# Kernel optimization log

Hardware: AMD Instinct MI355X
Metric: run time of the kernel (lower is better)

The kernel has to match this reference:

```python
import jax, jax.numpy as jnp
import numpy as np
import math

B, L, D = 2, 4096, 1024
K = D // 4


def _rotor(angles):
    # angles: [..., 6] -> scalar part s: [...], bivector part: [..., 6]
    mag = jnp.maximum(jnp.linalg.norm(angles, axis=-1), 1e-8)
    s = jnp.cos(mag)
    biv = (jnp.sin(mag) / mag)[..., None] * angles
    return s, biv


def _apply_rotor(s, biv, v):
    # s: [...], biv: [..., 6] (e12,e13,e14,e23,e24,e34), v: [..., 4]
    t12, t13, t14, t23, t24, t34 = (biv[..., i] for i in range(6))
    v1, v2, v3, v4 = (v[..., i] for i in range(4))
    s2 = s * s
    ts = 2.0 * s
    v1n = v1 * (s2 - t12 * t12 - t13 * t13 - t14 * t14) + ts * (v2 * t12 + v3 * t13 + v4 * t14)
    v2n = v2 * (s2 - t12 * t12 - t23 * t23 - t24 * t24) + ts * (-v1 * t12 + v3 * t23 + v4 * t24)
    v3n = v3 * (s2 - t13 * t13 - t23 * t23 - t34 * t34) + ts * (-v1 * t13 - v2 * t23 + v4 * t34)
    v4n = v4 * (s2 - t14 * t14 - t24 * t24 - t34 * t34) + ts * (-v1 * t14 - v2 * t24 - v3 * t34)
    return jnp.stack([v1n, v2n, v3n, v4n], axis=-1)


def _forward(x, wk1, bk1, wk2, bk2, wq1, bq1, wq2, bq2, wv, bv, ln_g, ln_b, wo, bo):
    b, l, d = x.shape
    k = d // 4
    gelu = lambda t: jax.nn.gelu(t, approximate=False)  # torch nn.GELU default = exact
    half_pi = math.pi / 2
    key_angles = (jnp.tanh(gelu(x @ wk1 + bk1) @ wk2 + bk2) * half_pi).reshape(b, l, k, 6)
    query_angles = (jnp.tanh(gelu(x @ wq1 + bq1) @ wq2 + bq2) * half_pi).reshape(b, l, k, 6)
    value = (x @ wv + bv).reshape(b, l, k, 4)
    ks, kb = _rotor(key_angles)
    qs, qb = _rotor(query_angles)
    rotated_value = _apply_rotor(ks, kb, value)          # [B,L,K,4]
    memory = jnp.cumsum(rotated_value, axis=1)            # running sum over sequence
    retrieved = _apply_rotor(qs, -qb, memory)             # reversed query rotor
    retrieved = retrieved.reshape(b, l, d)
    norm = jnp.sqrt(jnp.arange(1, l + 1, dtype=x.dtype))[None, :, None]
    r = retrieved / norm
    # LayerNorm (eps=1e-5) then Linear
    mu = jnp.mean(r, axis=-1, keepdims=True)
    var = jnp.mean((r - mu) ** 2, axis=-1, keepdims=True)
    rn = (r - mu) / jnp.sqrt(var + 1e-5) * ln_g + ln_b
    return x + rn @ wo + bo


def setup_inputs() -> dict:
    key = jax.random.key(0)
    ks = jax.random.split(key, 8)
    lin = lambda k, fi, fo: (jax.random.normal(k, (fi, fo), jnp.float32) * 0.02)
    return {
        "x": jax.random.normal(ks[0], (B, L, D), jnp.float32),
        "wk1": lin(ks[1], D, D), "bk1": jnp.zeros((D,), jnp.float32),
        "wk2": lin(ks[2], D, K * 6), "bk2": jnp.zeros((K * 6,), jnp.float32),
        "wq1": lin(ks[3], D, D), "bq1": jnp.zeros((D,), jnp.float32),
        "wq2": lin(ks[4], D, K * 6), "bq2": jnp.zeros((K * 6,), jnp.float32),
        "wv": lin(ks[5], D, D), "bv": jnp.zeros((D,), jnp.float32),
        "ln_g": jnp.ones((D,), jnp.float32), "ln_b": jnp.zeros((D,), jnp.float32),
        "wo": lin(ks[6], D, D), "bo": jnp.zeros((D,), jnp.float32),
    }


def reference(x, wk1, bk1, wk2, bk2, wq1, bq1, wq2, bq2, wv, bv, ln_g, ln_b, wo, bo):
    return _forward(x, wk1, bk1, wk2, bk2, wq1, bq1, wq2, bq2, wv, bv, ln_g, ln_b, wo, bo)
```

## Files before the change

kernel.cpp:

```cpp
#include <hip/hip_runtime.h>
#include <hip/hip_bf16.h>
#include <math.h>

#define D_DIM 1024
#define L_DIM 4096
#define B_DIM 2
#define K_DIM 256
#define N6    1536
#define M_ROWS 8192
#define CHUNKS 256
#define CHUNK_LEN 16
#define HALF_PI 1.57079632679489662f

typedef __attribute__((ext_vector_type(8))) short short8;
typedef __attribute__((ext_vector_type(4))) float f32x4;
typedef unsigned short us;

__device__ __forceinline__ void gload_lds16(const void* g, void* l) {
    __builtin_amdgcn_global_load_lds(
        (const __attribute__((address_space(1))) unsigned int*)g,
        (__attribute__((address_space(3))) unsigned int*)l,
        16, 0, 0);
}
__device__ __forceinline__ float bf2f(us u) {
    union { unsigned int i; float f; } c; c.i = ((unsigned int)u) << 16; return c.f;
}
__device__ __forceinline__ us f2bf(float v) {
    __hip_bfloat16 h = __float2bfloat16(v);
    return *(us*)&h;
}
__device__ __forceinline__ float tanh_fast(float x) {
    return 1.0f - 2.0f / (1.0f + __expf(2.0f * x));
}
__device__ __forceinline__ float gelu_fast(float x) {
    return x / (1.0f + __expf(-1.5957691216057308f * x * (1.0f + 0.044715f * x * x)));
}

__device__ __forceinline__ void rotor_from_angles(const float a[6], float& s, float b[6]) {
    float m2 = a[0]*a[0] + a[1]*a[1] + a[2]*a[2] + a[3]*a[3] + a[4]*a[4] + a[5]*a[5];
    float mag = fmaxf(sqrtf(m2), 1e-8f);
    s = __cosf(mag);
    float f = __sinf(mag) / mag;
    #pragma unroll
    for (int i = 0; i < 6; ++i) b[i] = f * a[i];
}
__device__ __forceinline__ void apply_rotor(float s, const float b[6], const float v[4], float o[4]) {
    float t12 = b[0], t13 = b[1], t14 = b[2], t23 = b[3], t24 = b[4], t34 = b[5];
    float v1 = v[0], v2 = v[1], v3 = v[2], v4 = v[3];
    float s2 = s * s;
    float ts = 2.0f * s;
    o[0] = v1 * (s2 - t12*t12 - t13*t13 - t14*t14) + ts * ( v2*t12 + v3*t13 + v4*t14);
    o[1] = v2 * (s2 - t12*t12 - t23*t23 - t24*t24) + ts * (-v1*t12 + v3*t23 + v4*t24);
    o[2] = v3 * (s2 - t13*t13 - t23*t23 - t34*t34) + ts * (-v1*t13 - v2*t23 + v4*t34);
    o[3] = v4 * (s2 - t14*t14 - t24*t24 - t34*t34) + ts * (-v1*t14 - v2*t24 - v3*t34);
}

__global__ __launch_bounds__(256)
void pack_b4(const float* __restrict__ w0, const float* __restrict__ w1,
             const float* __restrict__ w2, const float* __restrict__ w3,
             us* __restrict__ o0, us* __restrict__ o1,
             us* __restrict__ o2, us* __restrict__ o3, int Kd, int N)
{
    const float* W = (blockIdx.z == 0) ? w0 : (blockIdx.z == 1) ? w1 : (blockIdx.z == 2) ? w2 : w3;
    us* O = (blockIdx.z == 0) ? o0 : (blockIdx.z == 1) ? o1 : (blockIdx.z == 2) ? o2 : o3;
    if (W == nullptr) return;
    int nf = blockIdx.x;
    int kt = blockIdx.y * 4 + (threadIdx.x >> 6);
    int l = threadIdx.x & 63;
    int n = nf * 16 + (l & 15);
    int k0 = kt * 32 + (l >> 4) * 8;
    union { us u[8]; uint4 v; } pk;
    #pragma unroll
    for (int j = 0; j < 8; ++j)
        pk.u[j] = f2bf(W[(size_t)(k0 + j) * N + n]);
    *(uint4*)(O + ((size_t)nf * (Kd >> 5) + kt) * 512 + l * 8) = pk.v;
}

__global__ __launch_bounds__(256)
void cvt_bf16_kernel(const float* __restrict__ in, us* __restrict__ out)
{
    size_t i = ((size_t)blockIdx.x * 256 + threadIdx.x) * 8;
    float4 v0 = *(const float4*)(in + i);
    float4 v1 = *(const float4*)(in + i + 4);
    union { us u[8]; uint4 v; } pk;
    pk.u[0] = f2bf(v0.x); pk.u[1] = f2bf(v0.y); pk.u[2] = f2bf(v0.z); pk.u[3] = f2bf(v0.w);
    pk.u[4] = f2bf(v1.x); pk.u[5] = f2bf(v1.y); pk.u[6] = f2bf(v1.z); pk.u[7] = f2bf(v1.w);
    *(uint4*)(out + i) = pk.v;
}

__device__ __forceinline__ int xcd_swz(int bid, int nwg) {
    int cpx = nwg >> 3;
    return (bid & 7) * cpx + (bid >> 3);
}


#define GBAR()  do { __builtin_amdgcn_s_barrier(); __builtin_amdgcn_sched_barrier(0); } while (0)

__device__ __forceinline__ void gemm128_core(
    const us* __restrict__ Ab, const us* __restrict__ Bp, int Kd, int bn,
    short* lds, f32x4 (&acc)[4][4])
{
    const int tid = threadIdx.x;
    const int l = tid & 63, w = tid >> 6;
    const int wr = w >> 1, wc = w & 1;
    const int fr = l & 15, fq = l >> 4;
    const int nkt = Kd >> 5;

    #pragma unroll
    for (int i = 0; i < 4; ++i)
        #pragma unroll
        for (int j = 0; j < 4; ++j)
            acc[i][j] = (f32x4){0.f, 0.f, 0.f, 0.f};

    const us* bptr[4];
    #pragma unroll
    for (int ni = 0; ni < 4; ++ni)
        bptr[ni] = Bp + ((size_t)((bn >> 4) + wc * 4 + ni) * nkt) * 512 + l * 8;

    const int sr = tid >> 2, su = tid & 3;
    const int slu = su ^ ((sr >> 1) & 3);
    const us* gA0 = Ab + (size_t)sr * Kd + slu * 8;
    const us* gA1 = gA0 + (size_t)64 * Kd;

    const int swu = (fq ^ ((fr >> 1) & 3)) * 8;
    const int arow = (wr * 64 + fr) * 32 + swu;

    gload_lds16(gA0,      lds + tid * 8);
    gload_lds16(gA1,      lds + 2048 + tid * 8);
    gload_lds16(gA0 + 32, lds + 4096 + tid * 8);
    gload_lds16(gA1 + 32, lds + 6144 + tid * 8);
    gload_lds16(gA0 + 64, lds + 8192 + tid * 8);
    gload_lds16(gA1 + 64, lds + 10240 + tid * 8);
    asm volatile("s_waitcnt vmcnt(4)" ::: "memory");
    short8 bA[4], bB[4];
    #pragma unroll
    for (int ni = 0; ni < 4; ++ni) bA[ni] = *(const short8*)(bptr[ni]);
    #pragma unroll
    for (int ni = 0; ni < 4; ++ni) bB[ni] = *(const short8*)(bptr[ni] + 512);
    GBAR();

    for (int t = 0; t < nkt; t += 2) {
        {
            const int cb = (t % 3) * 4096;
            const int sb = ((t + 2) % 3) * 4096;
            const int tp = (t + 2 < nkt) ? (t + 2) : (nkt - 1);
            short8 a[4];
            #pragma unroll
            for (int mi = 0; mi < 4; ++mi)
                a[mi] = *(const short8*)(lds + cb + arow + mi * 512);
            gload_lds16(gA0 + tp * 32, lds + sb + tid * 8);
            gload_lds16(gA1 + tp * 32, lds + sb + 2048 + tid * 8);
            __builtin_amdgcn_s_setprio(1);
            #pragma unroll
            for (int mi = 0; mi < 4; ++mi)
                #pragma unroll
                for (int ni = 0; ni < 4; ++ni)
                    acc[mi][ni] = __builtin_amdgcn_mfma_f32_16x16x32_bf16(bA[ni], a[mi], acc[mi][ni], 0, 0, 0);
            __builtin_amdgcn_sched_barrier(0);
            __builtin_amdgcn_s_setprio(0);
            #pragma unroll
            for (int ni = 0; ni < 4; ++ni)
                bA[ni] = *(const short8*)(bptr[ni] + (size_t)tp * 512);
            asm volatile("s_waitcnt vmcnt(6)" ::: "memory");
            GBAR();
        }
        {
            const int t1 = t + 1;
            const int cb = (t1 % 3) * 4096;
            const int sb = ((t1 + 2) % 3) * 4096;
            const int tp = (t1 + 2 < nkt) ? (t1 + 2) : (nkt - 1);
            short8 a[4];
            #pragma unroll
            for (int mi = 0; mi < 4; ++mi)
                a[mi] = *(const short8*)(lds + cb + arow + mi * 512);
            gload_lds16(gA0 + tp * 32, lds + sb + tid * 8);
            gload_lds16(gA1 + tp * 32, lds + sb + 2048 + tid * 8);
            __builtin_amdgcn_s_setprio(1);
            #pragma unroll
            for (int mi = 0; mi < 4; ++mi)
                #pragma unroll
                for (int ni = 0; ni < 4; ++ni)
                    acc[mi][ni] = __builtin_amdgcn_mfma_f32_16x16x32_bf16(bB[ni], a[mi], acc[mi][ni], 0, 0, 0);
            __builtin_amdgcn_sched_barrier(0);
            __builtin_amdgcn_s_setprio(0);
            #pragma unroll
            for (int ni = 0; ni < 4; ++ni)
                bB[ni] = *(const short8*)(bptr[ni] + (size_t)tp * 512);
            asm volatile("s_waitcnt vmcnt(6)" ::: "memory");
            GBAR();
        }
    }
}

__global__ __launch_bounds__(256, 3)
void gemm_fused3(const us* __restrict__ xb,
                 const us* __restrict__ w0p, const us* __restrict__ w1p, const us* __restrict__ w2p,
                 const float* __restrict__ b0, const float* __restrict__ b1, const float* __restrict__ b2,
                 us* __restrict__ o0, us* __restrict__ o1, us* __restrict__ o2)
{
    __shared__ short lds[12288];
    const int wg = xcd_swz(blockIdx.x, 1536);
    const int bm = (wg / 24) * 128;
    const int col = wg % 24;
    const int r = col >> 3;
    const int bn = (col & 7) * 128;
    const us* Bp = (r == 0) ? w0p : (r == 1) ? w1p : w2p;
    const float* bias = (r == 0) ? b0 : (r == 1) ? b1 : b2;
    us* outp = (r == 0) ? o0 : (r == 1) ? o1 : o2;
    f32x4 acc[4][4];
    gemm128_core(xb + (size_t)bm * D_DIM, Bp, D_DIM, bn, lds, acc);
    const int l = threadIdx.x & 63, w = threadIdx.x >> 6;
    const int wr = w >> 1, wc = w & 1, fr = l & 15, fq = l >> 4;
    #pragma unroll
    for (int mi = 0; mi < 4; ++mi) {
        int row = bm + wr * 64 + mi * 16 + fr;
        #pragma unroll
        for (int ni = 0; ni < 4; ++ni) {
            int c0 = bn + wc * 64 + ni * 16 + fq * 4;
            float4 bs = *(const float4*)(bias + c0);
            float v0 = acc[mi][ni][0] + bs.x, v1 = acc[mi][ni][1] + bs.y;
            float v2 = acc[mi][ni][2] + bs.z, v3 = acc[mi][ni][3] + bs.w;
            if (r < 2) { v0 = gelu_fast(v0); v1 = gelu_fast(v1); v2 = gelu_fast(v2); v3 = gelu_fast(v3); }
            ushort4 pk; pk.x = f2bf(v0); pk.y = f2bf(v1); pk.z = f2bf(v2); pk.w = f2bf(v3);
            *(ushort4*)(outp + (size_t)row * D_DIM + c0) = pk;
        }
    }
}

__global__ __launch_bounds__(256, 3)
void gemm_angles(const us* __restrict__ Hk, const us* __restrict__ Hq,
                 const us* __restrict__ wk2p, const us* __restrict__ wq2p,
                 const float* __restrict__ bk2, const float* __restrict__ bq2,
                 us* __restrict__ ak, us* __restrict__ aq)
{
    __shared__ short lds[12288];
    const int wg = xcd_swz(blockIdx.x, 1536);
    const int z = wg / 768;
    const int rem = wg % 768;
    const int bm = (rem / 12) * 128;
    const int bn = (rem % 12) * 128;
    const us* A  = z ? Hq : Hk;
    const us* Bp = z ? wq2p : wk2p;
    const float* bias = z ? bq2 : bk2;
    us* outp = z ? aq : ak;
    f32x4 acc[4][4];
    gemm128_core(A + (size_t)bm * D_DIM, Bp, D_DIM, bn, lds, acc);
    const int l = threadIdx.x & 63, w = threadIdx.x >> 6;
    const int wr = w >> 1, wc = w & 1, fr = l & 15, fq = l >> 4;
    #pragma unroll
    for (int mi = 0; mi < 4; ++mi) {
        int row = bm + wr * 64 + mi * 16 + fr;
        #pragma unroll
        for (int ni = 0; ni < 4; ++ni) {
            int c0 = bn + wc * 64 + ni * 16 + fq * 4;
            float4 bs = *(const float4*)(bias + c0);
            ushort4 pk;
            pk.x = f2bf(tanh_fast(acc[mi][ni][0] + bs.x) * HALF_PI);
            pk.y = f2bf(tanh_fast(acc[mi][ni][1] + bs.y) * HALF_PI);
            pk.z = f2bf(tanh_fast(acc[mi][ni][2] + bs.z) * HALF_PI);
            pk.w = f2bf(tanh_fast(acc[mi][ni][3] + bs.w) * HALF_PI);
            *(ushort4*)(outp + (size_t)row * N6 + c0) = pk;
        }
    }
}

__global__ __launch_bounds__(256, 3)
void gemm_final(const us* __restrict__ rn, const us* __restrict__ wop,
                const float* __restrict__ bo, const float* __restrict__ x,
                float* __restrict__ out)
{
    __shared__ short lds[12288];
    const int wg = xcd_swz(blockIdx.x, 512);
    const int bm = (wg / 8) * 128;
    const int bn = (wg % 8) * 128;
    f32x4 acc[4][4];
    gemm128_core(rn + (size_t)bm * D_DIM, wop, D_DIM, bn, lds, acc);
    const int l = threadIdx.x & 63, w = threadIdx.x >> 6;
    const int wr = w >> 1, wc = w & 1, fr = l & 15, fq = l >> 4;
    #pragma unroll
    for (int mi = 0; mi < 4; ++mi) {
        int row = bm + wr * 64 + mi * 16 + fr;
        #pragma unroll
        for (int ni = 0; ni < 4; ++ni) {
            int c0 = bn + wc * 64 + ni * 16 + fq * 4;
            size_t off = (size_t)row * D_DIM + c0;
            float4 bs = *(const float4*)(bo + c0);
            float4 rx = *(const float4*)(x + off);
            float4 o;
            o.x = acc[mi][ni][0] + bs.x + rx.x;
            o.y = acc[mi][ni][1] + bs.y + rx.y;
            o.z = acc[mi][ni][2] + bs.z + rx.z;
            o.w = acc[mi][ni][3] + bs.w + rx.w;
            *(float4*)(out + off) = o;
        }
    }
}

__global__ __launch_bounds__(256)
void rot_chunk_sum(us* __restrict__ value, const us* __restrict__ ak,
                   float4* __restrict__ sums)
{
    int bc = blockIdx.x;
    int b = bc >> 8, c = bc & 255;
    int k = threadIdx.x;
    float4 acc = make_float4(0.f, 0.f, 0.f, 0.f);
    size_t row0 = (size_t)b * L_DIM + c * CHUNK_LEN;
    for (int i = 0; i < CHUNK_LEN; ++i) {
        size_t row = row0 + i;
        ushort4 uv = *(const ushort4*)(value + row * D_DIM + k * 4);
        const unsigned int* ap = (const unsigned int*)(ak + row * N6 + k * 6);
        unsigned int a0 = ap[0], a1 = ap[1], a2 = ap[2];
        float a[6] = { bf2f(a0 & 0xffff), bf2f(a0 >> 16), bf2f(a1 & 0xffff),
                       bf2f(a1 >> 16), bf2f(a2 & 0xffff), bf2f(a2 >> 16) };
        float s, bb[6];
        rotor_from_angles(a, s, bb);
        float v[4] = {bf2f(uv.x), bf2f(uv.y), bf2f(uv.z), bf2f(uv.w)}, o[4];
        apply_rotor(s, bb, v, o);
        ushort4 pkr;
        pkr.x = f2bf(o[0]); pkr.y = f2bf(o[1]); pkr.z = f2bf(o[2]); pkr.w = f2bf(o[3]);
        *(ushort4*)(value + row * D_DIM + k * 4) = pkr;
        acc.x += bf2f(pkr.x); acc.y += bf2f(pkr.y); acc.z += bf2f(pkr.z); acc.w += bf2f(pkr.w);
    }
    sums[(size_t)bc * 256 + k] = acc;
}

__global__ __launch_bounds__(256)
void scan_chunks_kernel(const float4* __restrict__ sums, float4* __restrict__ carry)
{
    int b = blockIdx.x >> 8;
    int k = blockIdx.x & 255;
    int c = threadIdx.x;
    __shared__ float4 sh[CHUNKS];
    float4 v = sums[((size_t)(b * CHUNKS + c)) * 256 + k];
    sh[c] = v;
    __syncthreads();
    for (int off = 1; off < CHUNKS; off <<= 1) {
        float4 t = make_float4(0.f, 0.f, 0.f, 0.f);
        if (c >= off) t = sh[c - off];
        __syncthreads();
        v.x += t.x; v.y += t.y; v.z += t.z; v.w += t.w;
        sh[c] = v;
        __syncthreads();
    }
    float4 ex = make_float4(0.f, 0.f, 0.f, 0.f);
    if (c > 0) ex = sh[c - 1];
    carry[((size_t)(b * CHUNKS + c)) * 256 + k] = ex;
}

__global__ __launch_bounds__(256)
void scan_apply_ln(const us* __restrict__ value, const us* __restrict__ aq,
                   const float4* __restrict__ carry,
                   const float* __restrict__ g, const float* __restrict__ bta,
                   us* __restrict__ rn)
{
    int bc = blockIdx.x;
    int b = bc >> 8, c = bc & 255;
    int k = threadIdx.x;
    int wv = k >> 6, lane = k & 63;
    float4 run = carry[(size_t)bc * 256 + k];
    float4 gv = *(const float4*)(g + k * 4);
    float4 bv = *(const float4*)(bta + k * 4);
    __shared__ float reds[4], redq[4];
    for (int i = 0; i < CHUNK_LEN; ++i) {
        int l = c * CHUNK_LEN + i;
        size_t row = (size_t)b * L_DIM + l;
        ushort4 uv = *(const ushort4*)(value + row * D_DIM + k * 4);
        run.x += bf2f(uv.x); run.y += bf2f(uv.y); run.z += bf2f(uv.z); run.w += bf2f(uv.w);
        const unsigned int* aqp = (const unsigned int*)(aq + row * N6 + k * 6);
        unsigned int qa0 = aqp[0], qa1 = aqp[1], qa2 = aqp[2];
        float aq6[6] = { bf2f(qa0 & 0xffff), bf2f(qa0 >> 16), bf2f(qa1 & 0xffff),
                         bf2f(qa1 >> 16), bf2f(qa2 & 0xffff), bf2f(qa2 >> 16) };
        float qs, qb[6];
        rotor_from_angles(aq6, qs, qb);
        #pragma unroll
        for (int t = 0; t < 6; ++t) qb[t] = -qb[t];
        float mem[4] = {run.x, run.y, run.z, run.w}, o2[4];
        apply_rotor(qs, qb, mem, o2);
        float inv = rsqrtf((float)(l + 1));
        o2[0] *= inv; o2[1] *= inv; o2[2] *= inv; o2[3] *= inv;
        float sm = o2[0] + o2[1] + o2[2] + o2[3];
        float qm = o2[0]*o2[0] + o2[1]*o2[1] + o2[2]*o2[2] + o2[3]*o2[3];
        #pragma unroll
        for (int off = 1; off < 64; off <<= 1) {
            sm += __shfl_xor(sm, off);
            qm += __shfl_xor(qm, off);
        }
        if (lane == 0) { reds[wv] = sm; redq[wv] = qm; }
        __syncthreads();
        sm = reds[0] + reds[1] + reds[2] + reds[3];
        qm = redq[0] + redq[1] + redq[2] + redq[3];
        float mu = sm * (1.0f / 1024.0f);
        float var = qm * (1.0f / 1024.0f) - mu * mu;
        float rstd = rsqrtf(var + 1e-5f);
        ushort4 pk;
        pk.x = f2bf((o2[0] - mu) * rstd * gv.x + bv.x);
        pk.y = f2bf((o2[1] - mu) * rstd * gv.y + bv.y);
        pk.z = f2bf((o2[2] - mu) * rstd * gv.z + bv.z);
        pk.w = f2bf((o2[3] - mu) * rstd * gv.w + bv.w);
        *(ushort4*)(rn + row * D_DIM + k * 4) = pk;
        __syncthreads();
    }
}

extern "C" void kernel_launch(void* const* d_in, const int* in_sizes, int n_in,
                              void* d_out, int out_size, void* d_ws, size_t ws_size,
                              hipStream_t stream)
{
    const float* x   = (const float*)d_in[0];
    const float* wk1 = (const float*)d_in[1];
    const float* bk1 = (const float*)d_in[2];
    const float* wk2 = (const float*)d_in[3];
    const float* bk2 = (const float*)d_in[4];
    const float* wq1 = (const float*)d_in[5];
    const float* bq1 = (const float*)d_in[6];
    const float* wq2 = (const float*)d_in[7];
    const float* bq2 = (const float*)d_in[8];
    const float* wv  = (const float*)d_in[9];
    const float* bv  = (const float*)d_in[10];
    const float* lng = (const float*)d_in[11];
    const float* lnb = (const float*)d_in[12];
    const float* wo  = (const float*)d_in[13];
    const float* bo  = (const float*)d_in[14];
    float* out = (float*)d_out;

    char* ws = (char*)d_ws;
    us* xb    = (us*)(ws);
    us* Hk    = (us*)(ws + (16ull  << 20));
    us* Hq    = (us*)(ws + (32ull  << 20));
    us* val   = (us*)(ws + (48ull  << 20));
    us* ak    = (us*)(ws + (64ull  << 20));
    us* aq    = (us*)(ws + (88ull  << 20));
    float4* sums  = (float4*)(ws + (112ull << 20));
    float4* carry = (float4*)(ws + (114ull << 20));
    us* wk1p  = (us*)(ws + (116ull << 20));
    us* wq1p  = (us*)(ws + (118ull << 20));
    us* wvp   = (us*)(ws + (120ull << 20));
    us* wop   = (us*)(ws + (122ull << 20));
    us* wk2p  = (us*)(ws + (124ull << 20));
    us* wq2p  = (us*)(ws + (127ull << 20));
    us* rn    = xb;

    dim3 blk(256);
    pack_b4<<<dim3(D_DIM / 16, D_DIM / 128, 4), blk, 0, stream>>>(
        wk1, wq1, wv, wo, wk1p, wq1p, wvp, wop, D_DIM, D_DIM);
    pack_b4<<<dim3(N6 / 16, D_DIM / 128, 2), blk, 0, stream>>>(
        wk2, wq2, nullptr, nullptr, wk2p, wq2p, nullptr, nullptr, D_DIM, N6);
    cvt_bf16_kernel<<<dim3(M_ROWS * D_DIM / (256 * 8)), blk, 0, stream>>>(x, xb);

    gemm_fused3<<<dim3(1536), blk, 0, stream>>>(
        xb, wk1p, wq1p, wvp, bk1, bq1, bv, Hk, Hq, val);
    gemm_angles<<<dim3(1536), blk, 0, stream>>>(
        Hk, Hq, wk2p, wq2p, bk2, bq2, ak, aq);
    rot_chunk_sum<<<dim3(B_DIM * CHUNKS), blk, 0, stream>>>(val, ak, sums);
    scan_chunks_kernel<<<dim3(B_DIM * K_DIM), blk, 0, stream>>>(sums, carry);
    scan_apply_ln<<<dim3(B_DIM * CHUNKS), blk, 0, stream>>>(val, aq, carry, lng, lnb, rn);
    gemm_final<<<dim3(512), blk, 0, stream>>>(rn, wop, bo, x, out);
}
```

Baseline: 229.3 us.

## Replace 128x128 GEMMs with 256x256 eight-wave tiles using transposed bf16 weights

The first-layer fused GEMM and the angle GEMM move from a 128x128, 4-wave tile to a 256x256, 8-wave tile. The new tile double-buffers K=64 slices in 128KB of dynamic LDS with an XOR swizzle, and interleaves four MFMA quadrants with staged global-to-LDS loads. Weights are now transposed and converted into plain N-major bf16 by a shared-memory transpose kernel, replacing the fragment-packed layout. The aim is more operand reuse and fewer global/LDS loads per FLOP. The costs are a 384-block grid that fills 256 CUs unevenly, occupancy limited to about one block per CU by LDS, and hipFuncSetAttribute calls on every launch.

```diff
diff --git a/kernel.cpp b/kernel.cpp
--- a/kernel.cpp
+++ b/kernel.cpp
@@ -56,14 +56,29 @@
 }
 
 __global__ __launch_bounds__(256)
-void pack_b4(const float* __restrict__ w0, const float* __restrict__ w1,
-             const float* __restrict__ w2, const float* __restrict__ w3,
-             us* __restrict__ o0, us* __restrict__ o1,
-             us* __restrict__ o2, us* __restrict__ o3, int Kd, int N)
+void transpose_cvt4(const float* __restrict__ w0, const float* __restrict__ w1,
+                    const float* __restrict__ w2, const float* __restrict__ w3,
+                    us* __restrict__ o0, us* __restrict__ o1,
+                    us* __restrict__ o2, us* __restrict__ o3, int Kd, int N)
 {
     const float* W = (blockIdx.z == 0) ? w0 : (blockIdx.z == 1) ? w1 : (blockIdx.z == 2) ? w2 : w3;
-    us* O = (blockIdx.z == 0) ? o0 : (blockIdx.z == 1) ? o1 : (blockIdx.z == 2) ? o2 : o3;
+    us* Wt = (blockIdx.z == 0) ? o0 : (blockIdx.z == 1) ? o1 : (blockIdx.z == 2) ? o2 : o3;
     if (W == nullptr) return;
+    __shared__ float sh[32][33];
+    int n0 = blockIdx.x * 32, k0 = blockIdx.y * 32;
+    int tx = threadIdx.x & 31, ty = threadIdx.x >> 5;
+    #pragma unroll
+    for (int i = 0; i < 32; i += 8)
+        sh[ty + i][tx] = W[(size_t)(k0 + ty + i) * N + n0 + tx];
+    __syncthreads();
+    #pragma unroll
+    for (int i = 0; i < 32; i += 8)
+        Wt[(size_t)(n0 + ty + i) * Kd + k0 + tx] = f2bf(sh[tx][ty + i]);
+}
+
+__global__ __launch_bounds__(256)
+void pack_b1(const float* __restrict__ W, us* __restrict__ O, int Kd, int N)
+{
     int nf = blockIdx.x;
     int kt = blockIdx.y * 4 + (threadIdx.x >> 6);
     int l = threadIdx.x & 63;
@@ -93,8 +108,214 @@
     return (bid & 7) * cpx + (bid >> 3);
 }
 
-
 #define GBAR()  do { __builtin_amdgcn_s_barrier(); __builtin_amdgcn_sched_barrier(0); } while (0)
+#define LGKM0() do { asm volatile("s_waitcnt lgkmcnt(0)" ::: "memory"); __builtin_amdgcn_sched_barrier(0); } while (0)
+
+
+__device__ __forceinline__ void gemm256_core(
+    const us* __restrict__ Ab, const us* __restrict__ Bb, int Kd,
+    short* lds, f32x4 (&acc)[8][4])
+{
+    const int tid = threadIdx.x;
+    const int l = tid & 63, w = tid >> 6;
+    const int wm = w >> 2, wn = w & 3;
+    const int fr = l & 15, fq = l >> 4, fr7 = fr & 7;
+    const int w16 = w * 16, sr = l >> 3;
+    const int gu = (l & 7) ^ sr;
+    const int nkt = Kd >> 6;
+
+    #pragma unroll
+    for (int i = 0; i < 8; ++i)
+        #pragma unroll
+        for (int j = 0; j < 4; ++j)
+            acc[i][j] = (f32x4){0.f, 0.f, 0.f, 0.f};
+
+    short* buf0 = lds;
+    short* buf1 = lds + 32768;
+
+    auto STAGE = [&](const us* gbase, int GR, int kt, short* half) {
+        gload_lds16(gbase + (size_t)(GR + w16 + sr) * Kd + kt * 64 + gu * 8,
+                    half + w16 * 64 + l * 8);
+        gload_lds16(gbase + (size_t)(GR + w16 + 8 + sr) * Kd + kt * 64 + gu * 8,
+                    half + (w16 + 8) * 64 + l * 8);
+    };
+
+    STAGE(Ab, 0,   0, buf0 + 0);
+    STAGE(Ab, 128, 0, buf0 + 8192);
+    STAGE(Bb, 0,   0, buf0 + 16384);
+    STAGE(Bb, 128, 0, buf0 + 24576);
+    STAGE(Bb, 0,   1, buf1 + 16384);
+    STAGE(Ab, 0,   1, buf1 + 0);
+    asm volatile("s_waitcnt vmcnt(4)" ::: "memory");
+    GBAR();
+
+    const int aoff = wm * 8192;
+    const int boff = 16384 + (wn >> 1) * 8192;
+    const int brow0 = (wn & 1) * 64;
+
+    short8 aR[4][2], bLo[2][2], bHi[2][2];
+
+    for (int t = 0; t < nkt; ++t) {
+        short* cb = (t & 1) ? buf1 : buf0;
+        short* ob = (t & 1) ? buf0 : buf1;
+        const int t1 = (t + 1 < nkt) ? t + 1 : nkt - 1;
+        const int t2 = (t + 2 < nkt) ? t + 2 : nkt - 1;
+        short* abuf = cb + aoff;
+        short* bbuf = cb + boff;
+
+        #pragma unroll
+        for (int mi = 0; mi < 4; ++mi)
+            #pragma unroll
+            for (int ks = 0; ks < 2; ++ks)
+                aR[mi][ks] = *(const short8*)(abuf + (mi * 16 + fr) * 64 + (((ks * 4 + fq) ^ fr7) * 8));
+        #pragma unroll
+        for (int ni = 0; ni < 2; ++ni)
+            #pragma unroll
+            for (int ks = 0; ks < 2; ++ks)
+                bLo[ni][ks] = *(const short8*)(bbuf + (brow0 + ni * 16 + fr) * 64 + (((ks * 4 + fq) ^ fr7) * 8));
+        STAGE(Ab, 128, t1, ob + 8192);
+        __builtin_amdgcn_s_barrier();
+        LGKM0();
+        __builtin_amdgcn_s_setprio(1);
+        #pragma unroll
+        for (int mi = 0; mi < 4; ++mi)
+            #pragma unroll
+            for (int ni = 0; ni < 2; ++ni)
+                #pragma unroll
+                for (int ks = 0; ks < 2; ++ks)
+                    acc[mi][ni] = __builtin_amdgcn_mfma_f32_16x16x32_bf16(bLo[ni][ks], aR[mi][ks], acc[mi][ni], 0, 0, 0);
+        __builtin_amdgcn_sched_barrier(0);
+        __builtin_amdgcn_s_setprio(0);
+        GBAR();
+
+        #pragma unroll
+        for (int ni = 0; ni < 2; ++ni)
+            #pragma unroll
+            for (int ks = 0; ks < 2; ++ks)
+                bHi[ni][ks] = *(const short8*)(bbuf + (brow0 + (ni + 2) * 16 + fr) * 64 + (((ks * 4 + fq) ^ fr7) * 8));
+        STAGE(Bb, 128, t1, ob + 24576);
+        __builtin_amdgcn_s_barrier();
+        LGKM0();
+        __builtin_amdgcn_s_setprio(1);
+        #pragma unroll
+        for (int mi = 0; mi < 4; ++mi)
+            #pragma unroll
+            for (int ni = 0; ni < 2; ++ni)
+                #pragma unroll
+                for (int ks = 0; ks < 2; ++ks)
+                    acc[mi][ni + 2] = __builtin_amdgcn_mfma_f32_16x16x32_bf16(bHi[ni][ks], aR[mi][ks], acc[mi][ni + 2], 0, 0, 0);
+        __builtin_amdgcn_sched_barrier(0);
+        __builtin_amdgcn_s_setprio(0);
+        GBAR();
+
+        #pragma unroll
+        for (int mi = 0; mi < 4; ++mi)
+            #pragma unroll
+            for (int ks = 0; ks < 2; ++ks)
+                aR[mi][ks] = *(const short8*)(abuf + ((mi + 4) * 16 + fr) * 64 + (((ks * 4 + fq) ^ fr7) * 8));
+        STAGE(Bb, 0, t2, cb + 16384);
+        __builtin_amdgcn_s_barrier();
+        LGKM0();
+        __builtin_amdgcn_s_setprio(1);
+        #pragma unroll
+        for (int mi = 0; mi < 4; ++mi)
+            #pragma unroll
+            for (int ni = 0; ni < 2; ++ni)
+                #pragma unroll
+                for (int ks = 0; ks < 2; ++ks)
+                    acc[mi + 4][ni + 2] = __builtin_amdgcn_mfma_f32_16x16x32_bf16(bHi[ni][ks], aR[mi][ks], acc[mi + 4][ni + 2], 0, 0, 0);
+        __builtin_amdgcn_sched_barrier(0);
+        __builtin_amdgcn_s_setprio(0);
+        GBAR();
+
+        STAGE(Ab, 0, t2, cb + 0);
+        GBAR();
+        __builtin_amdgcn_s_setprio(1);
+        #pragma unroll
+        for (int mi = 0; mi < 4; ++mi)
+            #pragma unroll
+            for (int ni = 0; ni < 2; ++ni)
+                #pragma unroll
+                for (int ks = 0; ks < 2; ++ks)
+                    acc[mi + 4][ni] = __builtin_amdgcn_mfma_f32_16x16x32_bf16(bLo[ni][ks], aR[mi][ks], acc[mi + 4][ni], 0, 0, 0);
+        __builtin_amdgcn_sched_barrier(0);
+        __builtin_amdgcn_s_setprio(0);
+        asm volatile("s_waitcnt vmcnt(4)" ::: "memory");
+        GBAR();
+    }
+}
+
+__global__ __launch_bounds__(512, 2)
+void gemm256_fused3(const us* __restrict__ xb,
+                    const us* __restrict__ w0t, const us* __restrict__ w1t, const us* __restrict__ w2t,
+                    const float* __restrict__ b0, const float* __restrict__ b1, const float* __restrict__ b2,
+                    us* __restrict__ o0, us* __restrict__ o1, us* __restrict__ o2)
+{
+    extern __shared__ short lds[];
+    const int wg = xcd_swz(blockIdx.x, 384);
+    const int bm = (wg / 12) * 256;
+    const int col = wg % 12;
+    const int r = col >> 2;
+    const int bn = (col & 3) * 256;
+    const us* Bt = (r == 0) ? w0t : (r == 1) ? w1t : w2t;
+    const float* bias = (r == 0) ? b0 : (r == 1) ? b1 : b2;
+    us* outp = (r == 0) ? o0 : (r == 1) ? o1 : o2;
+    f32x4 acc[8][4];
+    gemm256_core(xb + (size_t)bm * D_DIM, Bt + (size_t)bn * D_DIM, D_DIM, lds, acc);
+    const int l = threadIdx.x & 63, w = threadIdx.x >> 6;
+    const int wm = w >> 2, wn = w & 3, fr = l & 15, fq = l >> 4;
+    #pragma unroll
+    for (int mi = 0; mi < 8; ++mi) {
+        int row = bm + wm * 128 + mi * 16 + fr;
+        #pragma unroll
+        for (int ni = 0; ni < 4; ++ni) {
+            int c0 = bn + wn * 64 + ni * 16 + fq * 4;
+            float4 bs = *(const float4*)(bias + c0);
+            float v0 = acc[mi][ni][0] + bs.x, v1 = acc[mi][ni][1] + bs.y;
+            float v2 = acc[mi][ni][2] + bs.z, v3 = acc[mi][ni][3] + bs.w;
+            if (r < 2) { v0 = gelu_fast(v0); v1 = gelu_fast(v1); v2 = gelu_fast(v2); v3 = gelu_fast(v3); }
+            ushort4 pk; pk.x = f2bf(v0); pk.y = f2bf(v1); pk.z = f2bf(v2); pk.w = f2bf(v3);
+            *(ushort4*)(outp + (size_t)row * D_DIM + c0) = pk;
+        }
+    }
+}
+
+__global__ __launch_bounds__(512, 2)
+void gemm256_angles(const us* __restrict__ Hk, const us* __restrict__ Hq,
+                    const us* __restrict__ wk2t, const us* __restrict__ wq2t,
+                    const float* __restrict__ bk2, const float* __restrict__ bq2,
+                    us* __restrict__ ak, us* __restrict__ aq)
+{
+    extern __shared__ short lds[];
+    const int wg = xcd_swz(blockIdx.x, 384);
+    const int z = wg / 192;
+    const int rem = wg % 192;
+    const int bm = (rem / 6) * 256;
+    const int bn = (rem % 6) * 256;
+    const us* A  = z ? Hq : Hk;
+    const us* Bt = z ? wq2t : wk2t;
+    const float* bias = z ? bq2 : bk2;
+    us* outp = z ? aq : ak;
+    f32x4 acc[8][4];
+    gemm256_core(A + (size_t)bm * D_DIM, Bt + (size_t)bn * D_DIM, D_DIM, lds, acc);
+    const int l = threadIdx.x & 63, w = threadIdx.x >> 6;
+    const int wm = w >> 2, wn = w & 3, fr = l & 15, fq = l >> 4;
+    #pragma unroll
+    for (int mi = 0; mi < 8; ++mi) {
+        int row = bm + wm * 128 + mi * 16 + fr;
+        #pragma unroll
+        for (int ni = 0; ni < 4; ++ni) {
+            int c0 = bn + wn * 64 + ni * 16 + fq * 4;
+            float4 bs = *(const float4*)(bias + c0);
+            ushort4 pk;
+            pk.x = f2bf(tanh_fast(acc[mi][ni][0] + bs.x) * HALF_PI);
+            pk.y = f2bf(tanh_fast(acc[mi][ni][1] + bs.y) * HALF_PI);
+            pk.z = f2bf(tanh_fast(acc[mi][ni][2] + bs.z) * HALF_PI);
+            pk.w = f2bf(tanh_fast(acc[mi][ni][3] + bs.w) * HALF_PI);
+            *(ushort4*)(outp + (size_t)row * N6 + c0) = pk;
+        }
+    }
+}
 
 __device__ __forceinline__ void gemm128_core(
     const us* __restrict__ Ab, const us* __restrict__ Bp, int Kd, int bn,
@@ -188,78 +409,6 @@
                 bB[ni] = *(const short8*)(bptr[ni] + (size_t)tp * 512);
             asm volatile("s_waitcnt vmcnt(6)" ::: "memory");
             GBAR();
-        }
-    }
-}
-
-__global__ __launch_bounds__(256, 3)
-void gemm_fused3(const us* __restrict__ xb,
-                 const us* __restrict__ w0p, const us* __restrict__ w1p, const us* __restrict__ w2p,
-                 const float* __restrict__ b0, const float* __restrict__ b1, const float* __restrict__ b2,
-                 us* __restrict__ o0, us* __restrict__ o1, us* __restrict__ o2)
-{
-    __shared__ short lds[12288];
-    const int wg = xcd_swz(blockIdx.x, 1536);
-    const int bm = (wg / 24) * 128;
-    const int col = wg % 24;
-    const int r = col >> 3;
-    const int bn = (col & 7) * 128;
-    const us* Bp = (r == 0) ? w0p : (r == 1) ? w1p : w2p;
-    const float* bias = (r == 0) ? b0 : (r == 1) ? b1 : b2;
-    us* outp = (r == 0) ? o0 : (r == 1) ? o1 : o2;
-    f32x4 acc[4][4];
-    gemm128_core(xb + (size_t)bm * D_DIM, Bp, D_DIM, bn, lds, acc);
-    const int l = threadIdx.x & 63, w = threadIdx.x >> 6;
-    const int wr = w >> 1, wc = w & 1, fr = l & 15, fq = l >> 4;
-    #pragma unroll
-    for (int mi = 0; mi < 4; ++mi) {
-        int row = bm + wr * 64 + mi * 16 + fr;
-        #pragma unroll
-        for (int ni = 0; ni < 4; ++ni) {
-            int c0 = bn + wc * 64 + ni * 16 + fq * 4;
-            float4 bs = *(const float4*)(bias + c0);
-            float v0 = acc[mi][ni][0] + bs.x, v1 = acc[mi][ni][1] + bs.y;
-            float v2 = acc[mi][ni][2] + bs.z, v3 = acc[mi][ni][3] + bs.w;
-            if (r < 2) { v0 = gelu_fast(v0); v1 = gelu_fast(v1); v2 = gelu_fast(v2); v3 = gelu_fast(v3); }
-            ushort4 pk; pk.x = f2bf(v0); pk.y = f2bf(v1); pk.z = f2bf(v2); pk.w = f2bf(v3);
-            *(ushort4*)(outp + (size_t)row * D_DIM + c0) = pk;
-        }
-    }
-}
-
-__global__ __launch_bounds__(256, 3)
-void gemm_angles(const us* __restrict__ Hk, const us* __restrict__ Hq,
-                 const us* __restrict__ wk2p, const us* __restrict__ wq2p,
-                 const float* __restrict__ bk2, const float* __restrict__ bq2,
-                 us* __restrict__ ak, us* __restrict__ aq)
-{
-    __shared__ short lds[12288];
-    const int wg = xcd_swz(blockIdx.x, 1536);
-    const int z = wg / 768;
-    const int rem = wg % 768;
-    const int bm = (rem / 12) * 128;
-    const int bn = (rem % 12) * 128;
-    const us* A  = z ? Hq : Hk;
-    const us* Bp = z ? wq2p : wk2p;
-    const float* bias = z ? bq2 : bk2;
-    us* outp = z ? aq : ak;
-    f32x4 acc[4][4];
-    gemm128_core(A + (size_t)bm * D_DIM, Bp, D_DIM, bn, lds, acc);
-    const int l = threadIdx.x & 63, w = threadIdx.x >> 6;
-    const int wr = w >> 1, wc = w & 1, fr = l & 15, fq = l >> 4;
-    #pragma unroll
-    for (int mi = 0; mi < 4; ++mi) {
-        int row = bm + wr * 64 + mi * 16 + fr;
-        #pragma unroll
-        for (int ni = 0; ni < 4; ++ni) {
-            int c0 = bn + wc * 64 + ni * 16 + fq * 4;
-            float4 bs = *(const float4*)(bias + c0);
-            ushort4 pk;
-            pk.x = f2bf(tanh_fast(acc[mi][ni][0] + bs.x) * HALF_PI);
-            pk.y = f2bf(tanh_fast(acc[mi][ni][1] + bs.y) * HALF_PI);
-            pk.z = f2bf(tanh_fast(acc[mi][ni][2] + bs.z) * HALF_PI);
-            pk.w = f2bf(tanh_fast(acc[mi][ni][3] + bs.w) * HALF_PI);
-            *(ushort4*)(outp + (size_t)row * N6 + c0) = pk;
         }
     }
 }
@@ -432,25 +581,32 @@
     us* aq    = (us*)(ws + (88ull  << 20));
     float4* sums  = (float4*)(ws + (112ull << 20));
     float4* carry = (float4*)(ws + (114ull << 20));
-    us* wk1p  = (us*)(ws + (116ull << 20));
-    us* wq1p  = (us*)(ws + (118ull << 20));
-    us* wvp   = (us*)(ws + (120ull << 20));
+    us* wk1t  = (us*)(ws + (116ull << 20));
+    us* wq1t  = (us*)(ws + (118ull << 20));
+    us* wvt   = (us*)(ws + (120ull << 20));
     us* wop   = (us*)(ws + (122ull << 20));
-    us* wk2p  = (us*)(ws + (124ull << 20));
-    us* wq2p  = (us*)(ws + (127ull << 20));
+    us* wk2t  = (us*)(ws + (124ull << 20));
+    us* wq2t  = (us*)(ws + (127ull << 20));
     us* rn    = xb;
 
+    hipFuncSetAttribute((const void*)gemm256_fused3,
+                        hipFuncAttributeMaxDynamicSharedMemorySize, 131072);
+    hipFuncSetAttribute((const void*)gemm256_angles,
+                        hipFuncAttributeMaxDynamicSharedMemorySize, 131072);
+
     dim3 blk(256);
-    pack_b4<<<dim3(D_DIM / 16, D_DIM / 128, 4), blk, 0, stream>>>(
-        wk1, wq1, wv, wo, wk1p, wq1p, wvp, wop, D_DIM, D_DIM);
-    pack_b4<<<dim3(N6 / 16, D_DIM / 128, 2), blk, 0, stream>>>(
-        wk2, wq2, nullptr, nullptr, wk2p, wq2p, nullptr, nullptr, D_DIM, N6);
+    transpose_cvt4<<<dim3(D_DIM / 32, D_DIM / 32, 3), blk, 0, stream>>>(
+        wk1, wq1, wv, nullptr, wk1t, wq1t, wvt, nullptr, D_DIM, D_DIM);
+    transpose_cvt4<<<dim3(N6 / 32, D_DIM / 32, 2), blk, 0, stream>>>(
+        wk2, wq2, nullptr, nullptr, wk2t, wq2t, nullptr, nullptr, D_DIM, N6);
+    pack_b1<<<dim3(D_DIM / 16, D_DIM / 128), blk, 0, stream>>>(wo, wop, D_DIM, D_DIM);
     cvt_bf16_kernel<<<dim3(M_ROWS * D_DIM / (256 * 8)), blk, 0, stream>>>(x, xb);
 
-    gemm_fused3<<<dim3(1536), blk, 0, stream>>>(
-        xb, wk1p, wq1p, wvp, bk1, bq1, bv, Hk, Hq, val);
-    gemm_angles<<<dim3(1536), blk, 0, stream>>>(
-        Hk, Hq, wk2p, wq2p, bk2, bq2, ak, aq);
+    dim3 blk512(512);
+    gemm256_fused3<<<dim3(384), blk512, 131072, stream>>>(
+        xb, wk1t, wq1t, wvt, bk1, bq1, bv, Hk, Hq, val);
+    gemm256_angles<<<dim3(384), blk512, 131072, stream>>>(
+        Hk, Hq, wk2t, wq2t, bk2, bq2, ak, aq);
     rot_chunk_sum<<<dim3(B_DIM * CHUNKS), blk, 0, stream>>>(val, ak, sums);
     scan_chunks_kernel<<<dim3(B_DIM * K_DIM), blk, 0, stream>>>(sums, carry);
     scan_apply_ln<<<dim3(B_DIM * CHUNKS), blk, 0, stream>>>(val, aq, carry, lng, lnb, rn);
```

New measurement: 241.8 us. +5.5%, slower.

## Double GEMM K-step to 64 per LDS stage with wider swizzle

Applied to the files above, without the earlier changes.

The shared bf16 GEMM core now stages 64-wide K tiles of A in LDS instead of 32, so each triple-buffered stage holds 128x64 elements. Each stage issues two MFMA sweeps, and B fragments are prefetched two K-subtiles at a time. The goal is to halve the number of barriers and loop iterations per K, amortising synchronisation and load-issue overhead. In exchange LDS per block doubles to 48KB, which may limit occupancy under launch_bounds(256,3), and more registers are needed for the B fragments.

```diff
diff --git a/kernel.cpp b/kernel.cpp
--- a/kernel.cpp
+++ b/kernel.cpp
@@ -93,8 +93,8 @@
     return (bid & 7) * cpx + (bid >> 3);
 }
 
-
 #define GBAR()  do { __builtin_amdgcn_s_barrier(); __builtin_amdgcn_sched_barrier(0); } while (0)
+
 
 __device__ __forceinline__ void gemm128_core(
     const us* __restrict__ Ab, const us* __restrict__ Bp, int Kd, int bn,
@@ -104,7 +104,8 @@
     const int l = tid & 63, w = tid >> 6;
     const int wr = w >> 1, wc = w & 1;
     const int fr = l & 15, fq = l >> 4;
-    const int nkt = Kd >> 5;
+    const int nkt = Kd >> 6;
+    const int nt32 = Kd >> 5;
 
     #pragma unroll
     for (int i = 0; i < 4; ++i)
@@ -115,78 +116,114 @@
     const us* bptr[4];
     #pragma unroll
     for (int ni = 0; ni < 4; ++ni)
-        bptr[ni] = Bp + ((size_t)((bn >> 4) + wc * 4 + ni) * nkt) * 512 + l * 8;
-
-    const int sr = tid >> 2, su = tid & 3;
-    const int slu = su ^ ((sr >> 1) & 3);
-    const us* gA0 = Ab + (size_t)sr * Kd + slu * 8;
-    const us* gA1 = gA0 + (size_t)64 * Kd;
-
-    const int swu = (fq ^ ((fr >> 1) & 3)) * 8;
-    const int arow = (wr * 64 + fr) * 32 + swu;
-
-    gload_lds16(gA0,      lds + tid * 8);
-    gload_lds16(gA1,      lds + 2048 + tid * 8);
-    gload_lds16(gA0 + 32, lds + 4096 + tid * 8);
-    gload_lds16(gA1 + 32, lds + 6144 + tid * 8);
-    gload_lds16(gA0 + 64, lds + 8192 + tid * 8);
-    gload_lds16(gA1 + 64, lds + 10240 + tid * 8);
+        bptr[ni] = Bp + ((size_t)((bn >> 4) + wc * 4 + ni) * nt32) * 512 + l * 8;
+
+    const us* gA[4];
+    int dsto[4];
+    #pragma unroll
+    for (int j = 0; j < 4; ++j) {
+        int idx = tid + j * 256;
+        int row = idx >> 3, u = idx & 7;
+        int lu = u ^ (row & 7);
+        gA[j] = Ab + (size_t)row * Kd + lu * 8;
+        dsto[j] = idx * 8;
+    }
+
+    const int sw0 = ((fq) ^ (fr & 7)) * 8;
+    const int sw1 = ((4 + fq) ^ (fr & 7)) * 8;
+    const int rowb = (wr * 64 + fr) * 64;
+
+    #pragma unroll
+    for (int j = 0; j < 4; ++j) gload_lds16(gA[j], lds + dsto[j]);
+    #pragma unroll
+    for (int j = 0; j < 4; ++j) gload_lds16(gA[j] + 64, lds + 8192 + dsto[j]);
+    short8 bA[4][2], bB[4][2];
+    #pragma unroll
+    for (int ni = 0; ni < 4; ++ni)
+        #pragma unroll
+        for (int ks = 0; ks < 2; ++ks) {
+            bA[ni][ks] = *(const short8*)(bptr[ni] + (0 + ks) * 512);
+            bB[ni][ks] = *(const short8*)(bptr[ni] + (2 + ks) * 512);
+        }
     asm volatile("s_waitcnt vmcnt(4)" ::: "memory");
-    short8 bA[4], bB[4];
-    #pragma unroll
-    for (int ni = 0; ni < 4; ++ni) bA[ni] = *(const short8*)(bptr[ni]);
-    #pragma unroll
-    for (int ni = 0; ni < 4; ++ni) bB[ni] = *(const short8*)(bptr[ni] + 512);
     GBAR();
 
     for (int t = 0; t < nkt; t += 2) {
         {
-            const int cb = (t % 3) * 4096;
-            const int sb = ((t + 2) % 3) * 4096;
+            const int cb = (t % 3) * 8192;
+            const int sb = ((t + 2) % 3) * 8192;
             const int tp = (t + 2 < nkt) ? (t + 2) : (nkt - 1);
             short8 a[4];
             #pragma unroll
             for (int mi = 0; mi < 4; ++mi)
-                a[mi] = *(const short8*)(lds + cb + arow + mi * 512);
-            gload_lds16(gA0 + tp * 32, lds + sb + tid * 8);
-            gload_lds16(gA1 + tp * 32, lds + sb + 2048 + tid * 8);
+                a[mi] = *(const short8*)(lds + cb + rowb + mi * 1024 + sw0);
+            #pragma unroll
+            for (int j = 0; j < 4; ++j)
+                gload_lds16(gA[j] + tp * 64, lds + sb + dsto[j]);
             __builtin_amdgcn_s_setprio(1);
             #pragma unroll
             for (int mi = 0; mi < 4; ++mi)
                 #pragma unroll
                 for (int ni = 0; ni < 4; ++ni)
-                    acc[mi][ni] = __builtin_amdgcn_mfma_f32_16x16x32_bf16(bA[ni], a[mi], acc[mi][ni], 0, 0, 0);
+                    acc[mi][ni] = __builtin_amdgcn_mfma_f32_16x16x32_bf16(bA[ni][0], a[mi], acc[mi][ni], 0, 0, 0);
             __builtin_amdgcn_sched_barrier(0);
             __builtin_amdgcn_s_setprio(0);
             #pragma unroll
+            for (int mi = 0; mi < 4; ++mi)
+                a[mi] = *(const short8*)(lds + cb + rowb + mi * 1024 + sw1);
+            __builtin_amdgcn_s_setprio(1);
+            #pragma unroll
+            for (int mi = 0; mi < 4; ++mi)
+                #pragma unroll
+                for (int ni = 0; ni < 4; ++ni)
+                    acc[mi][ni] = __builtin_amdgcn_mfma_f32_16x16x32_bf16(bA[ni][1], a[mi], acc[mi][ni], 0, 0, 0);
+            __builtin_amdgcn_sched_barrier(0);
+            __builtin_amdgcn_s_setprio(0);
+            #pragma unroll
             for (int ni = 0; ni < 4; ++ni)
-                bA[ni] = *(const short8*)(bptr[ni] + (size_t)tp * 512);
-            asm volatile("s_waitcnt vmcnt(6)" ::: "memory");
+                #pragma unroll
+                for (int ks = 0; ks < 2; ++ks)
+                    bA[ni][ks] = *(const short8*)(bptr[ni] + (size_t)(2 * tp + ks) * 512);
+            asm volatile("s_waitcnt vmcnt(12)" ::: "memory");
             GBAR();
         }
         {
             const int t1 = t + 1;
-            const int cb = (t1 % 3) * 4096;
-            const int sb = ((t1 + 2) % 3) * 4096;
+            const int cb = (t1 % 3) * 8192;
+            const int sb = ((t1 + 2) % 3) * 8192;
             const int tp = (t1 + 2 < nkt) ? (t1 + 2) : (nkt - 1);
             short8 a[4];
             #pragma unroll
             for (int mi = 0; mi < 4; ++mi)
-                a[mi] = *(const short8*)(lds + cb + arow + mi * 512);
-            gload_lds16(gA0 + tp * 32, lds + sb + tid * 8);
-            gload_lds16(gA1 + tp * 32, lds + sb + 2048 + tid * 8);
+                a[mi] = *(const short8*)(lds + cb + rowb + mi * 1024 + sw0);
+            #pragma unroll
+            for (int j = 0; j < 4; ++j)
+                gload_lds16(gA[j] + tp * 64, lds + sb + dsto[j]);
             __builtin_amdgcn_s_setprio(1);
             #pragma unroll
             for (int mi = 0; mi < 4; ++mi)
                 #pragma unroll
                 for (int ni = 0; ni < 4; ++ni)
-                    acc[mi][ni] = __builtin_amdgcn_mfma_f32_16x16x32_bf16(bB[ni], a[mi], acc[mi][ni], 0, 0, 0);
+                    acc[mi][ni] = __builtin_amdgcn_mfma_f32_16x16x32_bf16(bB[ni][0], a[mi], acc[mi][ni], 0, 0, 0);
             __builtin_amdgcn_sched_barrier(0);
             __builtin_amdgcn_s_setprio(0);
             #pragma unroll
+            for (int mi = 0; mi < 4; ++mi)
+                a[mi] = *(const short8*)(lds + cb + rowb + mi * 1024 + sw1);
+            __builtin_amdgcn_s_setprio(1);
+            #pragma unroll
+            for (int mi = 0; mi < 4; ++mi)
+                #pragma unroll
+                for (int ni = 0; ni < 4; ++ni)
+                    acc[mi][ni] = __builtin_amdgcn_mfma_f32_16x16x32_bf16(bB[ni][1], a[mi], acc[mi][ni], 0, 0, 0);
+            __builtin_amdgcn_sched_barrier(0);
+            __builtin_amdgcn_s_setprio(0);
+            #pragma unroll
             for (int ni = 0; ni < 4; ++ni)
-                bB[ni] = *(const short8*)(bptr[ni] + (size_t)tp * 512);
-            asm volatile("s_waitcnt vmcnt(6)" ::: "memory");
+                #pragma unroll
+                for (int ks = 0; ks < 2; ++ks)
+                    bB[ni][ks] = *(const short8*)(bptr[ni] + (size_t)(2 * tp + ks) * 512);
+            asm volatile("s_waitcnt vmcnt(12)" ::: "memory");
             GBAR();
         }
     }
@@ -198,7 +235,7 @@
                  const float* __restrict__ b0, const float* __restrict__ b1, const float* __restrict__ b2,
                  us* __restrict__ o0, us* __restrict__ o1, us* __restrict__ o2)
 {
-    __shared__ short lds[12288];
+    __shared__ short lds[24576];
     const int wg = xcd_swz(blockIdx.x, 1536);
     const int bm = (wg / 24) * 128;
     const int col = wg % 24;
@@ -233,7 +270,7 @@
                  const float* __restrict__ bk2, const float* __restrict__ bq2,
                  us* __restrict__ ak, us* __restrict__ aq)
 {
-    __shared__ short lds[12288];
+    __shared__ short lds[24576];
     const int wg = xcd_swz(blockIdx.x, 1536);
     const int z = wg / 768;
     const int rem = wg % 768;
@@ -269,7 +306,7 @@
                 const float* __restrict__ bo, const float* __restrict__ x,
                 float* __restrict__ out)
 {
-    __shared__ short lds[12288];
+    __shared__ short lds[24576];
     const int wg = xcd_swz(blockIdx.x, 512);
     const int bm = (wg / 8) * 128;
     const int bn = (wg % 8) * 128;
```

Result: slower. 259.1 us (+13.0%).

## Store hidden activations in MFMA-packed layout and run angle GEMM without LDS

Applied to the files above, without the earlier changes.

The first fused GEMM now writes the GELU hidden activations Hk/Hq in the same fragment-packed layout used for the weights, so each lane's 16-byte MFMA operand is contiguous. The angle GEMM then uses a new LDS-free core that loads A and B fragments straight from global memory into registers, double-buffered across two k-steps, with no barriers. This removes LDS staging and synchronisation from the second GEMM. The cost is more global traffic per block, since operands are no longer shared through LDS, plus scattered partial-line stores in the first GEMM's epilogue.

```diff
diff --git a/kernel.cpp b/kernel.cpp
--- a/kernel.cpp
+++ b/kernel.cpp
@@ -55,6 +55,7 @@
     o[3] = v4 * (s2 - t14*t14 - t24*t24 - t34*t34) + ts * (-v1*t14 - v2*t24 - v3*t34);
 }
 
+
 __global__ __launch_bounds__(256)
 void pack_b4(const float* __restrict__ w0, const float* __restrict__ w1,
              const float* __restrict__ w2, const float* __restrict__ w3,
@@ -93,7 +94,6 @@
     return (bid & 7) * cpx + (bid >> 3);
 }
 
-
 #define GBAR()  do { __builtin_amdgcn_s_barrier(); __builtin_amdgcn_sched_barrier(0); } while (0)
 
 __device__ __forceinline__ void gemm128_core(
@@ -190,6 +190,78 @@
             GBAR();
         }
     }
+}
+
+__device__ __forceinline__ void gemm128p_core(
+    const us* __restrict__ Ap, const us* __restrict__ Bp, int nkt,
+    int bm, int bn, f32x4 (&acc)[4][4])
+{
+    const int tid = threadIdx.x;
+    const int l = tid & 63, w = tid >> 6;
+    const int wr = w >> 1, wc = w & 1;
+
+    #pragma unroll
+    for (int i = 0; i < 4; ++i)
+        #pragma unroll
+        for (int j = 0; j < 4; ++j)
+            acc[i][j] = (f32x4){0.f, 0.f, 0.f, 0.f};
+
+    const us* aptr[4];
+    const us* bptr[4];
+    #pragma unroll
+    for (int mi = 0; mi < 4; ++mi)
+        aptr[mi] = Ap + ((size_t)((bm >> 4) + wr * 4 + mi) * nkt) * 512 + l * 8;
+    #pragma unroll
+    for (int ni = 0; ni < 4; ++ni)
+        bptr[ni] = Bp + ((size_t)((bn >> 4) + wc * 4 + ni) * nkt) * 512 + l * 8;
+
+    short8 a0[4], b0[4], a1[4], b1[4];
+    #pragma unroll
+    for (int i = 0; i < 4; ++i) {
+        a0[i] = *(const short8*)(aptr[i]);
+        b0[i] = *(const short8*)(bptr[i]);
+        a1[i] = *(const short8*)(aptr[i] + 512);
+        b1[i] = *(const short8*)(bptr[i] + 512);
+    }
+
+    for (int t = 0; t < nkt; t += 2) {
+        const int tp0 = (t + 2 < nkt) ? (t + 2) : (nkt - 1);
+        const int tp1 = (t + 3 < nkt) ? (t + 3) : (nkt - 1);
+        __builtin_amdgcn_s_setprio(1);
+        #pragma unroll
+        for (int mi = 0; mi < 4; ++mi)
+            #pragma unroll
+            for (int ni = 0; ni < 4; ++ni)
+                acc[mi][ni] = __builtin_amdgcn_mfma_f32_16x16x32_bf16(b0[ni], a0[mi], acc[mi][ni], 0, 0, 0);
+        __builtin_amdgcn_s_setprio(0);
+        #pragma unroll
+        for (int i = 0; i < 4; ++i) {
+            a0[i] = *(const short8*)(aptr[i] + (size_t)tp0 * 512);
+            b0[i] = *(const short8*)(bptr[i] + (size_t)tp0 * 512);
+        }
+        __builtin_amdgcn_s_setprio(1);
+        #pragma unroll
+        for (int mi = 0; mi < 4; ++mi)
+            #pragma unroll
+            for (int ni = 0; ni < 4; ++ni)
+                acc[mi][ni] = __builtin_amdgcn_mfma_f32_16x16x32_bf16(b1[ni], a1[mi], acc[mi][ni], 0, 0, 0);
+        __builtin_amdgcn_s_setprio(0);
+        #pragma unroll
+        for (int i = 0; i < 4; ++i) {
+            a1[i] = *(const short8*)(aptr[i] + (size_t)tp1 * 512);
+            b1[i] = *(const short8*)(bptr[i] + (size_t)tp1 * 512);
+        }
+    }
+}
+
+__device__ __forceinline__ void pack_store4(us* __restrict__ P, int nkt,
+                                            int row, int c0, ushort4 v)
+{
+    int mf = row >> 4;
+    int kt = c0 >> 5;
+    int lp = (row & 15) | (((c0 >> 3) & 3) << 4);
+    int j0 = c0 & 7;
+    *(ushort4*)(P + ((size_t)mf * nkt + kt) * 512 + lp * 8 + j0) = v;
 }
 
 __global__ __launch_bounds__(256, 3)
@@ -222,29 +294,29 @@
             float v2 = acc[mi][ni][2] + bs.z, v3 = acc[mi][ni][3] + bs.w;
             if (r < 2) { v0 = gelu_fast(v0); v1 = gelu_fast(v1); v2 = gelu_fast(v2); v3 = gelu_fast(v3); }
             ushort4 pk; pk.x = f2bf(v0); pk.y = f2bf(v1); pk.z = f2bf(v2); pk.w = f2bf(v3);
-            *(ushort4*)(outp + (size_t)row * D_DIM + c0) = pk;
+            if (r < 2) pack_store4(outp, 32, row, c0, pk);
+            else       *(ushort4*)(outp + (size_t)row * D_DIM + c0) = pk;
         }
     }
 }
 
 __global__ __launch_bounds__(256, 3)
-void gemm_angles(const us* __restrict__ Hk, const us* __restrict__ Hq,
+void gemm_angles(const us* __restrict__ Hkp, const us* __restrict__ Hqp,
                  const us* __restrict__ wk2p, const us* __restrict__ wq2p,
                  const float* __restrict__ bk2, const float* __restrict__ bq2,
                  us* __restrict__ ak, us* __restrict__ aq)
 {
-    __shared__ short lds[12288];
     const int wg = xcd_swz(blockIdx.x, 1536);
     const int z = wg / 768;
     const int rem = wg % 768;
     const int bm = (rem / 12) * 128;
     const int bn = (rem % 12) * 128;
-    const us* A  = z ? Hq : Hk;
+    const us* Ap = z ? Hqp : Hkp;
     const us* Bp = z ? wq2p : wk2p;
     const float* bias = z ? bq2 : bk2;
     us* outp = z ? aq : ak;
     f32x4 acc[4][4];
-    gemm128_core(A + (size_t)bm * D_DIM, Bp, D_DIM, bn, lds, acc);
+    gemm128p_core(Ap, Bp, 32, bm, bn, acc);
     const int l = threadIdx.x & 63, w = threadIdx.x >> 6;
     const int wr = w >> 1, wc = w & 1, fr = l & 15, fq = l >> 4;
     #pragma unroll
@@ -425,8 +497,8 @@
 
     char* ws = (char*)d_ws;
     us* xb    = (us*)(ws);
-    us* Hk    = (us*)(ws + (16ull  << 20));
-    us* Hq    = (us*)(ws + (32ull  << 20));
+    us* Hkp   = (us*)(ws + (16ull  << 20));
+    us* Hqp   = (us*)(ws + (32ull  << 20));
     us* val   = (us*)(ws + (48ull  << 20));
     us* ak    = (us*)(ws + (64ull  << 20));
     us* aq    = (us*)(ws + (88ull  << 20));
@@ -448,9 +520,9 @@
     cvt_bf16_kernel<<<dim3(M_ROWS * D_DIM / (256 * 8)), blk, 0, stream>>>(x, xb);
 
     gemm_fused3<<<dim3(1536), blk, 0, stream>>>(
-        xb, wk1p, wq1p, wvp, bk1, bq1, bv, Hk, Hq, val);
+        xb, wk1p, wq1p, wvp, bk1, bq1, bv, Hkp, Hqp, val);
     gemm_angles<<<dim3(1536), blk, 0, stream>>>(
-        Hk, Hq, wk2p, wq2p, bk2, bq2, ak, aq);
+        Hkp, Hqp, wk2p, wq2p, bk2, bq2, ak, aq);
     rot_chunk_sum<<<dim3(B_DIM * CHUNKS), blk, 0, stream>>>(val, ak, sums);
     scan_chunks_kernel<<<dim3(B_DIM * K_DIM), blk, 0, stream>>>(sums, carry);
     scan_apply_ln<<<dim3(B_DIM * CHUNKS), blk, 0, stream>>>(val, aq, carry, lng, lnb, rn);
```

Result: slower. 238.6 us (+4.0%).
